# Optimization experiments

Hardware: AMD Instinct MI355X
Metric: run time of the kernel (lower is better)

The kernel has to match this reference:

```python
import jax, jax.numpy as jnp
import numpy as np

B, N, E, H = 4, 2048, 512, 8
D = E // H  # head dim = 64


def setup_inputs() -> dict:
    key = jax.random.key(0)
    ks = jax.random.split(key, 5)
    s = 1.0 / np.sqrt(E)
    return {
        "x": jax.random.normal(ks[0], (B, N, E), dtype=jnp.float32),
        "Wk": jax.random.normal(ks[1], (E, E), dtype=jnp.float32) * s,
        "bk": jax.random.normal(ks[2], (E,), dtype=jnp.float32) * s,
        "Wv": jax.random.normal(ks[3], (E, E), dtype=jnp.float32) * s,
        "bv": jax.random.normal(ks[4], (E,), dtype=jnp.float32) * s,
    }


def reference(x, Wk, bk, Wv, bv):
    b, n, e = x.shape
    # Linear projections (torch Linear: y = x @ W.T + b), split into heads.
    keys = (x @ Wk.T + bk).reshape(b, n, H, D).transpose(0, 2, 1, 3)    # b h n d
    values = (x @ Wv.T + bv).reshape(b, n, H, D).transpose(0, 2, 1, 3)  # b h n d
    # Q = K self-attention: scores [b, h, n, n]
    dotprod = jnp.einsum('bhnd,bhmd->bhnm', keys, keys)
    # softmax over last axis, then unusual POST-softmax scaling by sqrt(emb)
    att = jax.nn.softmax(dotprod, axis=-1) / jnp.sqrt(jnp.asarray(e, x.dtype))
    # dropout p=0 -> identity
    out = jnp.einsum('bhnm,bhmd->bhnd', att, values)
    return out.transpose(0, 2, 1, 3).reshape(b, n, e)
```

## Files before the change

kernel.cpp:

```cpp
#include <hip/hip_runtime.h>

typedef __bf16 bf16_t;
typedef bf16_t bf16x8 __attribute__((ext_vector_type(8)));
typedef float f32x4 __attribute__((ext_vector_type(4)));

#define NSEQ 2048
#define EMB 512
#define HEADS 8
#define HD 64
#define BATCH 4
#define LOG2E 1.4426950408889634f

#define XELEMS (BATCH * NSEQ * EMB)
#define WELEMS (EMB * EMB)

#define MFMA16(a, b, c) __builtin_amdgcn_mfma_f32_16x16x32_bf16(a, b, c, 0, 0, 0)


__global__ __launch_bounds__(256) void convert_kernel(
    const float* __restrict__ x, const float* __restrict__ Wk,
    const float* __restrict__ Wv, bf16_t* __restrict__ xb)
{
  const int i = blockIdx.x * 256 + threadIdx.x;
  const float* src;
  size_t off;
  bf16_t* dst;
  if (i < XELEMS / 8) {
    off = (size_t)i * 8;
    src = x;
    dst = xb + off;
  } else {
    const size_t e = (size_t)(i - XELEMS / 8) * 8;
    if (e < WELEMS) { src = Wk; off = e; }
    else            { src = Wv; off = e - WELEMS; }
    dst = xb + XELEMS + e;
  }
  const float4 a = *(const float4*)(src + off);
  const float4 b = *(const float4*)(src + off + 4);
  bf16x8 v;
  v[0] = (bf16_t)a.x; v[1] = (bf16_t)a.y; v[2] = (bf16_t)a.z; v[3] = (bf16_t)a.w;
  v[4] = (bf16_t)b.x; v[5] = (bf16_t)b.y; v[6] = (bf16_t)b.z; v[7] = (bf16_t)b.w;
  *(bf16x8*)dst = v;
}

__global__ __launch_bounds__(256, 2) void proj_kernel(
    const bf16_t* __restrict__ xb, const bf16_t* __restrict__ Wb,
    const float* __restrict__ bk, const float* __restrict__ bv,
    bf16_t* __restrict__ Kf, bf16_t* __restrict__ Vf)
{
  __shared__ union {
    struct {
      __align__(16) bf16_t A[128 * 64];
      __align__(16) bf16_t B[128 * 64];
    } s;
    __align__(16) bf16_t T[128][136];
  } u;

  const int t    = threadIdx.x;
  const int w    = t >> 6;
  const int lane = t & 63;
  const int quad = lane >> 4;
  const int l15  = lane & 15;
  const int wr   = w >> 1, wc = w & 1;
  const int m0   = blockIdx.x * 128;
  const int n0   = blockIdx.y * 128;
  const int zz   = (blockIdx.y >= 4);

  const int rsub = lane >> 3;
  const int cswz = (lane & 7) ^ rsub;

  auto stage = [&](int it) {
    const int kb = it * 64;
#pragma unroll
    for (int g = 0; g < 4; ++g) {
      const int r = w * 32 + g * 8;
      const bf16_t* gA = xb + (size_t)(m0 + r + rsub) * EMB + kb + cswz * 8;
      const bf16_t* gB = Wb + (size_t)(n0 + r + rsub) * EMB + kb + cswz * 8;
      __builtin_amdgcn_global_load_lds(
          (const __attribute__((address_space(1))) void*)gA,
          (__attribute__((address_space(3))) void*)&u.s.A[r * 64], 16, 0, 0);
      __builtin_amdgcn_global_load_lds(
          (const __attribute__((address_space(1))) void*)gB,
          (__attribute__((address_space(3))) void*)&u.s.B[r * 64], 16, 0, 0);
    }
  };
  auto rdA = [&](int R, int c) {
    return *(const bf16x8*)(&u.s.A[R * 64 + ((c ^ (R & 7)) << 3)]);
  };
  auto rdB = [&](int R, int c) {
    return *(const bf16x8*)(&u.s.B[R * 64 + ((c ^ (R & 7)) << 3)]);
  };

  f32x4 acc[4][4] = {};

  for (int it = 0; it < 8; ++it) {
    stage(it);
    __syncthreads();

    bf16x8 af[4][2], bfr[4][2];
#pragma unroll
    for (int mt = 0; mt < 4; ++mt)
#pragma unroll
      for (int kk = 0; kk < 2; ++kk)
        af[mt][kk] = rdA(wr * 64 + mt * 16 + l15, kk * 4 + quad);
#pragma unroll
    for (int nt = 0; nt < 4; ++nt)
#pragma unroll
      for (int kk = 0; kk < 2; ++kk)
        bfr[nt][kk] = rdB(wc * 64 + nt * 16 + l15, kk * 4 + quad);
#pragma unroll
    for (int kk = 0; kk < 2; ++kk)
#pragma unroll
      for (int mt = 0; mt < 4; ++mt)
#pragma unroll
        for (int nt = 0; nt < 4; ++nt)
          acc[mt][nt] = MFMA16(af[mt][kk], bfr[nt][kk], acc[mt][nt]);

    __syncthreads();
  }

#pragma unroll
  for (int mt = 0; mt < 4; ++mt) {
#pragma unroll
    for (int nt = 0; nt < 4; ++nt) {
      const int F = wc * 64 + nt * 16 + l15;
      const int c = n0 + F;
      const float bb = zz ? bv[c - 512] : bk[c];
#pragma unroll
      for (int reg = 0; reg < 4; ++reg) {
        const int R = wr * 64 + mt * 16 + quad * 4 + reg;
        const float v = acc[mt][nt][reg] + bb;
        if (!zz) u.T[R][F] = (bf16_t)v;
        else     u.T[F][R] = (bf16_t)v;
      }
    }
  }
  __syncthreads();

  if (!zz) {
#pragma unroll
    for (int i = 0; i < 8; ++i) {
      const int fi  = i * 4 + w;
      const int hL  = fi >> 4, kk = (fi >> 3) & 1, ktl = fi & 7;
      const bf16x8 v = *(const bf16x8*)(&u.T[ktl * 16 + l15][hL * 64 + kk * 32 + quad * 8]);
      const int gr = m0 + ktl * 16 + l15;
      const int b = gr >> 11, n = gr & (NSEQ - 1);
      const int bh = b * HEADS + (n0 >> 6) + hL;
      bf16_t* dst = Kf + (((size_t)(bh * 128 + (n >> 4)) * 2 + kk)) * 512 + lane * 8;
      *(bf16x8*)dst = v;
    }
  } else {
#pragma unroll
    for (int i = 0; i < 8; ++i) {
      const int fi   = i * 4 + w;
      const int hL   = fi >> 4, dt = (fi >> 2) & 3, k32l = fi & 3;
      const bf16_t* Trow = &u.T[hL * 64 + dt * 16 + l15][0];
      const int r0 = k32l * 32 + (quad >> 1) * 16 + (quad & 1) * 4;
      union { uint2 d2[2]; bf16x8 v; } vv;
      vv.d2[0] = *(const uint2*)(Trow + r0);
      vv.d2[1] = *(const uint2*)(Trow + r0 + 8);
      const int gr = m0 + k32l * 32;
      const int b = gr >> 11, n = gr & (NSEQ - 1);
      const int bh = b * HEADS + ((n0 - 512) >> 6) + hL;
      bf16_t* dst = Vf + (((size_t)(bh * 64 + (n >> 5)) * 4 + dt)) * 512 + lane * 8;
      *(bf16x8*)dst = vv.v;
    }
  }
}

__global__ __launch_bounds__(256, 2) void flash_kernel(
    const bf16_t* __restrict__ Kf, const bf16_t* __restrict__ Vf,
    float* __restrict__ out)
{
  __shared__ struct {
    __align__(16) float Cb[2][4096];
    __align__(16) float Lb[2][64][16];
  } u;

  const int t    = threadIdx.x;
  const int w    = t >> 6;
  const int lane = t & 63;
  const int quad = lane >> 4;
  const int l15  = lane & 15;
  const int rh   = w & 1;
  const int kh   = w >> 1;

  const int bh = blockIdx.x;
  const int b  = bh >> 3, h = bh & 7;
  const int rowbase = blockIdx.y * 128 + rh * 64;
  const int qtile   = rowbase >> 4;

  const bf16_t* __restrict__ Kb = Kf + (size_t)bh * 128 * 2 * 512;
  const bf16_t* __restrict__ Vb = Vf + (size_t)bh * 64 * 4 * 512;

  bf16x8 qf[4][2];
#pragma unroll
  for (int nt = 0; nt < 4; ++nt)
#pragma unroll
    for (int kk = 0; kk < 2; ++kk)
      qf[nt][kk] = *(const bf16x8*)(Kb + ((size_t)(qtile + nt) * 2 + kk) * 512 + lane * 8);

  float mlog[4];
#pragma unroll
  for (int nt = 0; nt < 4; ++nt) {
    float ss = 0.f;
#pragma unroll
    for (int kk = 0; kk < 2; ++kk)
#pragma unroll
      for (int j = 0; j < 8; ++j) {
        const float qv = (float)qf[nt][kk][j];
        ss = fmaf(qv, qv, ss);
      }
    ss += __shfl_xor(ss, 16, 64);
    ss += __shfl_xor(ss, 32, 64);
    mlog[nt] = ss * LOG2E;
  }

  bf16x8 ones;
#pragma unroll
  for (int j = 0; j < 8; ++j) ones[j] = (bf16_t)1.0f;

  f32x4 acco[4][4] = {};
  f32x4 accll[4]   = {};

  auto load_k = [&](int kt, bf16x8 (&dst)[2][2]) {
    const int kb = kt * 4 + kh * 2;
#pragma unroll
    for (int jt = 0; jt < 2; ++jt)
#pragma unroll
      for (int kk = 0; kk < 2; ++kk)
        dst[jt][kk] =
            *(const bf16x8*)(Kb + ((size_t)(kb + jt) * 2 + kk) * 512 + lane * 8);
  };

  auto body = [&](int kt, bf16x8 (&kcur)[2][2], bf16x8 (&knxt)[2][2]) {
    bf16x8 vf[4];
    const int v32 = kt * 2 + kh;
#pragma unroll
    for (int dt = 0; dt < 4; ++dt)
      vf[dt] = *(const bf16x8*)(Vb + ((size_t)v32 * 4 + dt) * 512 + lane * 8);

    f32x4 st[2][4] = {};
    __builtin_amdgcn_s_setprio(1);
#pragma unroll
    for (int kk = 0; kk < 2; ++kk)
#pragma unroll
      for (int jt = 0; jt < 2; ++jt)
#pragma unroll
        for (int nt = 0; nt < 4; ++nt)
          st[jt][nt] = MFMA16(kcur[jt][kk], qf[nt][kk], st[jt][nt]);
    __builtin_amdgcn_s_setprio(0);

    load_k(kt + 1 < NSEQ / 64 ? kt + 1 : kt, knxt);

    bf16x8 pf[4];
#pragma unroll
    for (int nt = 0; nt < 4; ++nt) {
      union { bf16_t h[2]; unsigned uu; } w00, w01, w10, w11;
      w00.h[0] = (bf16_t)__builtin_amdgcn_exp2f(fmaf(st[0][nt][0], LOG2E, -mlog[nt]));
      w00.h[1] = (bf16_t)__builtin_amdgcn_exp2f(fmaf(st[0][nt][1], LOG2E, -mlog[nt]));
      w01.h[0] = (bf16_t)__builtin_amdgcn_exp2f(fmaf(st[0][nt][2], LOG2E, -mlog[nt]));
      w01.h[1] = (bf16_t)__builtin_amdgcn_exp2f(fmaf(st[0][nt][3], LOG2E, -mlog[nt]));
      w10.h[0] = (bf16_t)__builtin_amdgcn_exp2f(fmaf(st[1][nt][0], LOG2E, -mlog[nt]));
      w10.h[1] = (bf16_t)__builtin_amdgcn_exp2f(fmaf(st[1][nt][1], LOG2E, -mlog[nt]));
      w11.h[0] = (bf16_t)__builtin_amdgcn_exp2f(fmaf(st[1][nt][2], LOG2E, -mlog[nt]));
      w11.h[1] = (bf16_t)__builtin_amdgcn_exp2f(fmaf(st[1][nt][3], LOG2E, -mlog[nt]));
      auto r0 = __builtin_amdgcn_permlane32_swap(w00.uu, w10.uu, false, false);
      auto r1 = __builtin_amdgcn_permlane32_swap(w01.uu, w11.uu, false, false);
      union { unsigned uw[4]; bf16x8 v; } pk;
      pk.uw[0] = r0[0]; pk.uw[1] = r1[0]; pk.uw[2] = r0[1]; pk.uw[3] = r1[1];
      pf[nt] = pk.v;
    }

    __builtin_amdgcn_s_setprio(1);
#pragma unroll
    for (int rt = 0; rt < 4; ++rt) {
      accll[rt] = MFMA16(pf[rt], ones, accll[rt]);
#pragma unroll
      for (int dt = 0; dt < 4; ++dt)
        acco[rt][dt] = MFMA16(pf[rt], vf[dt], acco[rt][dt]);
    }
    __builtin_amdgcn_s_setprio(0);
  };

  bf16x8 kA[2][2], kB[2][2];
  load_k(0, kA);
  for (int kt = 0; kt < NSEQ / 64; kt += 2) {
    body(kt,     kA, kB);
    body(kt + 1, kB, kA);
  }

  __syncthreads();
  if (kh == 1) {
#pragma unroll
    for (int rt = 0; rt < 4; ++rt) {
#pragma unroll
      for (int dt = 0; dt < 4; ++dt)
        *(f32x4*)(&u.Cb[rh][((rt * 4 + dt) * 64 + lane) * 4]) = acco[rt][dt];
      *(f32x4*)(&u.Lb[rh][lane][rt * 4]) = accll[rt];
    }
  }
  __syncthreads();
  if (kh == 0) {
#pragma unroll
    for (int rt = 0; rt < 4; ++rt) {
#pragma unroll
      for (int dt = 0; dt < 4; ++dt)
        acco[rt][dt] += *(const f32x4*)(&u.Cb[rh][((rt * 4 + dt) * 64 + lane) * 4]);
      accll[rt] += *(const f32x4*)(&u.Lb[rh][lane][rt * 4]);
    }

    const float SCL = 0.044194173824159216f;
#pragma unroll
    for (int rt = 0; rt < 4; ++rt)
#pragma unroll
      for (int reg = 0; reg < 4; ++reg) {
        const float f = SCL / accll[rt][reg];
        const int n = rowbase + rt * 16 + quad * 4 + reg;
#pragma unroll
        for (int dt = 0; dt < 4; ++dt)
          out[((size_t)(b * NSEQ + n)) * EMB + h * HD + dt * 16 + l15] =
              acco[rt][dt][reg] * f;
      }
  }
}

extern "C" void kernel_launch(void* const* d_in, const int* in_sizes, int n_in,
                              void* d_out, int out_size, void* d_ws, size_t ws_size,
                              hipStream_t stream) {
  const float* x  = (const float*)d_in[0];
  const float* Wk = (const float*)d_in[1];
  const float* bk = (const float*)d_in[2];
  const float* Wv = (const float*)d_in[3];
  const float* bv = (const float*)d_in[4];
  float* out = (float*)d_out;

  bf16_t* Kf = (bf16_t*)d_ws;
  bf16_t* Vf = Kf + (size_t)BATCH * HEADS * NSEQ * HD;

  bf16_t* xb = (bf16_t*)d_out;
  bf16_t* Wb = xb + XELEMS;

  convert_kernel<<<(XELEMS / 8 + 2 * WELEMS / 8) / 256, 256, 0, stream>>>(
      x, Wk, Wv, xb);

  dim3 pg(8192 / 128, 1024 / 128);
  proj_kernel<<<pg, 256, 0, stream>>>(xb, Wb, bk, bv, Kf, Vf);

  dim3 fg(BATCH * HEADS, NSEQ / 128);
  flash_kernel<<<fg, 256, 0, stream>>>(Kf, Vf, out);
}
```

Baseline: 131.0 us.

## Split flash keys across four waves per block and double-buffer projection tiles

The attention kernel now gives each block 64 query rows and has its four waves each process a quarter of the key sequence. Partial outputs and row sums are combined through shared memory in a two-step tree reduction, the grid is doubled, and the occupancy hint is raised to four blocks per SM. The goal is more concurrent blocks and better latency hiding. Separately, the projection GEMM double-buffers its LDS tiles so the next K-slice loads while the current one is multiplied. The tighter launch bound may cap registers and cause spills, and the reduction adds extra barriers.

```diff
diff --git a/kernel.cpp b/kernel.cpp
--- a/kernel.cpp
+++ b/kernel.cpp
@@ -50,8 +50,8 @@
 {
   __shared__ union {
     struct {
-      __align__(16) bf16_t A[128 * 64];
-      __align__(16) bf16_t B[128 * 64];
+      __align__(16) bf16_t A[2][128 * 64];
+      __align__(16) bf16_t B[2][128 * 64];
     } s;
     __align__(16) bf16_t T[128][136];
   } u;
@@ -69,7 +69,7 @@
   const int rsub = lane >> 3;
   const int cswz = (lane & 7) ^ rsub;
 
-  auto stage = [&](int it) {
+  auto stage = [&](int it, int bufi) {
     const int kb = it * 64;
 #pragma unroll
     for (int g = 0; g < 4; ++g) {
@@ -78,36 +78,39 @@
       const bf16_t* gB = Wb + (size_t)(n0 + r + rsub) * EMB + kb + cswz * 8;
       __builtin_amdgcn_global_load_lds(
           (const __attribute__((address_space(1))) void*)gA,
-          (__attribute__((address_space(3))) void*)&u.s.A[r * 64], 16, 0, 0);
+          (__attribute__((address_space(3))) void*)&u.s.A[bufi][r * 64], 16, 0, 0);
       __builtin_amdgcn_global_load_lds(
           (const __attribute__((address_space(1))) void*)gB,
-          (__attribute__((address_space(3))) void*)&u.s.B[r * 64], 16, 0, 0);
-    }
-  };
-  auto rdA = [&](int R, int c) {
-    return *(const bf16x8*)(&u.s.A[R * 64 + ((c ^ (R & 7)) << 3)]);
-  };
-  auto rdB = [&](int R, int c) {
-    return *(const bf16x8*)(&u.s.B[R * 64 + ((c ^ (R & 7)) << 3)]);
+          (__attribute__((address_space(3))) void*)&u.s.B[bufi][r * 64], 16, 0, 0);
+    }
+  };
+  auto rdA = [&](int bufi, int R, int c) {
+    return *(const bf16x8*)(&u.s.A[bufi][R * 64 + ((c ^ (R & 7)) << 3)]);
+  };
+  auto rdB = [&](int bufi, int R, int c) {
+    return *(const bf16x8*)(&u.s.B[bufi][R * 64 + ((c ^ (R & 7)) << 3)]);
   };
 
   f32x4 acc[4][4] = {};
 
+  stage(0, 0);
+  __syncthreads();
+
   for (int it = 0; it < 8; ++it) {
-    stage(it);
-    __syncthreads();
+    const int cur = it & 1;
+    if (it < 7) stage(it + 1, cur ^ 1);
 
     bf16x8 af[4][2], bfr[4][2];
 #pragma unroll
     for (int mt = 0; mt < 4; ++mt)
 #pragma unroll
       for (int kk = 0; kk < 2; ++kk)
-        af[mt][kk] = rdA(wr * 64 + mt * 16 + l15, kk * 4 + quad);
+        af[mt][kk] = rdA(cur, wr * 64 + mt * 16 + l15, kk * 4 + quad);
 #pragma unroll
     for (int nt = 0; nt < 4; ++nt)
 #pragma unroll
       for (int kk = 0; kk < 2; ++kk)
-        bfr[nt][kk] = rdB(wc * 64 + nt * 16 + l15, kk * 4 + quad);
+        bfr[nt][kk] = rdB(cur, wc * 64 + nt * 16 + l15, kk * 4 + quad);
 #pragma unroll
     for (int kk = 0; kk < 2; ++kk)
 #pragma unroll
@@ -168,7 +171,7 @@
   }
 }
 
-__global__ __launch_bounds__(256, 2) void flash_kernel(
+__global__ __launch_bounds__(256, 4) void flash_kernel(
     const bf16_t* __restrict__ Kf, const bf16_t* __restrict__ Vf,
     float* __restrict__ out)
 {
@@ -178,16 +181,14 @@
   } u;
 
   const int t    = threadIdx.x;
-  const int w    = t >> 6;
+  const int kq   = t >> 6;
   const int lane = t & 63;
   const int quad = lane >> 4;
   const int l15  = lane & 15;
-  const int rh   = w & 1;
-  const int kh   = w >> 1;
 
   const int bh = blockIdx.x;
   const int b  = bh >> 3, h = bh & 7;
-  const int rowbase = blockIdx.y * 128 + rh * 64;
+  const int rowbase = blockIdx.y * 64;
   const int qtile   = rowbase >> 4;
 
   const bf16_t* __restrict__ Kb = Kf + (size_t)bh * 128 * 2 * 512;
@@ -223,8 +224,8 @@
   f32x4 acco[4][4] = {};
   f32x4 accll[4]   = {};
 
-  auto load_k = [&](int kt, bf16x8 (&dst)[2][2]) {
-    const int kb = kt * 4 + kh * 2;
+  auto load_k = [&](int s, bf16x8 (&dst)[2][2]) {
+    const int kb = (kq * 16 + s) * 2;
 #pragma unroll
     for (int jt = 0; jt < 2; ++jt)
 #pragma unroll
@@ -233,9 +234,9 @@
             *(const bf16x8*)(Kb + ((size_t)(kb + jt) * 2 + kk) * 512 + lane * 8);
   };
 
-  auto body = [&](int kt, bf16x8 (&kcur)[2][2], bf16x8 (&knxt)[2][2]) {
+  auto body = [&](int s, bf16x8 (&kcur)[2][2], bf16x8 (&knxt)[2][2]) {
     bf16x8 vf[4];
-    const int v32 = kt * 2 + kh;
+    const int v32 = kq * 16 + s;
 #pragma unroll
     for (int dt = 0; dt < 4; ++dt)
       vf[dt] = *(const bf16x8*)(Vb + ((size_t)v32 * 4 + dt) * 512 + lane * 8);
@@ -251,7 +252,7 @@
           st[jt][nt] = MFMA16(kcur[jt][kk], qf[nt][kk], st[jt][nt]);
     __builtin_amdgcn_s_setprio(0);
 
-    load_k(kt + 1 < NSEQ / 64 ? kt + 1 : kt, knxt);
+    load_k(s + 1 < 16 ? s + 1 : s, knxt);
 
     bf16x8 pf[4];
 #pragma unroll
@@ -285,30 +286,39 @@
 
   bf16x8 kA[2][2], kB[2][2];
   load_k(0, kA);
-  for (int kt = 0; kt < NSEQ / 64; kt += 2) {
-    body(kt,     kA, kB);
-    body(kt + 1, kB, kA);
-  }
-
-  __syncthreads();
-  if (kh == 1) {
+  for (int s = 0; s < 16; s += 2) {
+    body(s,     kA, kB);
+    body(s + 1, kB, kA);
+  }
+
+  auto dump = [&](int slot) {
 #pragma unroll
     for (int rt = 0; rt < 4; ++rt) {
 #pragma unroll
       for (int dt = 0; dt < 4; ++dt)
-        *(f32x4*)(&u.Cb[rh][((rt * 4 + dt) * 64 + lane) * 4]) = acco[rt][dt];
-      *(f32x4*)(&u.Lb[rh][lane][rt * 4]) = accll[rt];
-    }
-  }
-  __syncthreads();
-  if (kh == 0) {
+        *(f32x4*)(&u.Cb[slot][((rt * 4 + dt) * 64 + lane) * 4]) = acco[rt][dt];
+      *(f32x4*)(&u.Lb[slot][lane][rt * 4]) = accll[rt];
+    }
+  };
+  auto gather = [&](int slot) {
 #pragma unroll
     for (int rt = 0; rt < 4; ++rt) {
 #pragma unroll
       for (int dt = 0; dt < 4; ++dt)
-        acco[rt][dt] += *(const f32x4*)(&u.Cb[rh][((rt * 4 + dt) * 64 + lane) * 4]);
-      accll[rt] += *(const f32x4*)(&u.Lb[rh][lane][rt * 4]);
-    }
+        acco[rt][dt] += *(const f32x4*)(&u.Cb[slot][((rt * 4 + dt) * 64 + lane) * 4]);
+      accll[rt] += *(const f32x4*)(&u.Lb[slot][lane][rt * 4]);
+    }
+  };
+
+  __syncthreads();
+  if (kq & 1) dump(kq >> 1);
+  __syncthreads();
+  if (!(kq & 1)) gather(kq >> 1);
+  __syncthreads();
+  if (kq == 2) dump(0);
+  __syncthreads();
+  if (kq == 0) {
+    gather(0);
 
     const float SCL = 0.044194173824159216f;
 #pragma unroll
@@ -347,6 +357,6 @@
   dim3 pg(8192 / 128, 1024 / 128);
   proj_kernel<<<pg, 256, 0, stream>>>(xb, Wb, bk, bv, Kf, Vf);
 
-  dim3 fg(BATCH * HEADS, NSEQ / 128);
+  dim3 fg(BATCH * HEADS, NSEQ / 64);
   flash_kernel<<<fg, 256, 0, stream>>>(Kf, Vf, out);
 }
```

Result: slower. 458.7 us (+250.1%).

## Prefetch projection tiles into registers and use padded LDS layout

Applied to the files above, without the earlier changes.

Swaps the direct global-to-LDS async loads with XOR swizzle for register prefetching. The next K-slice is loaded into registers while MFMAs run on the current one, then stored into a padded [2][128][40] LDS layout that avoids bank conflicts. This overlaps global load latency with compute inside the projection GEMM. In exchange it uses more registers and adds explicit LDS store instructions, which could lower occupancy.

```diff
diff --git a/kernel.cpp b/kernel.cpp
--- a/kernel.cpp
+++ b/kernel.cpp
@@ -50,8 +50,8 @@
 {
   __shared__ union {
     struct {
-      __align__(16) bf16_t A[128 * 64];
-      __align__(16) bf16_t B[128 * 64];
+      __align__(16) bf16_t A[2][128][40];
+      __align__(16) bf16_t B[2][128][40];
     } s;
     __align__(16) bf16_t T[128][136];
   } u;
@@ -66,58 +66,53 @@
   const int n0   = blockIdx.y * 128;
   const int zz   = (blockIdx.y >= 4);
 
-  const int rsub = lane >> 3;
-  const int cswz = (lane & 7) ^ rsub;
-
-  auto stage = [&](int it) {
-    const int kb = it * 64;
-#pragma unroll
-    for (int g = 0; g < 4; ++g) {
-      const int r = w * 32 + g * 8;
-      const bf16_t* gA = xb + (size_t)(m0 + r + rsub) * EMB + kb + cswz * 8;
-      const bf16_t* gB = Wb + (size_t)(n0 + r + rsub) * EMB + kb + cswz * 8;
-      __builtin_amdgcn_global_load_lds(
-          (const __attribute__((address_space(1))) void*)gA,
-          (__attribute__((address_space(3))) void*)&u.s.A[r * 64], 16, 0, 0);
-      __builtin_amdgcn_global_load_lds(
-          (const __attribute__((address_space(1))) void*)gB,
-          (__attribute__((address_space(3))) void*)&u.s.B[r * 64], 16, 0, 0);
+  const int sr = t >> 3;
+  const int sj = t & 7;
+  const int sb = sj >> 2, sc = (sj & 3) * 8;
+
+  bf16x8 pa[4], pb[4];
+  auto prefetch = [&](int k0) {
+#pragma unroll
+    for (int i = 0; i < 4; ++i) {
+      pa[i] = *(const bf16x8*)(xb + (size_t)(m0 + sr + i * 32) * EMB + k0 + sj * 8);
+      pb[i] = *(const bf16x8*)(Wb + (size_t)(n0 + sr + i * 32) * EMB + k0 + sj * 8);
     }
   };
-  auto rdA = [&](int R, int c) {
-    return *(const bf16x8*)(&u.s.A[R * 64 + ((c ^ (R & 7)) << 3)]);
-  };
-  auto rdB = [&](int R, int c) {
-    return *(const bf16x8*)(&u.s.B[R * 64 + ((c ^ (R & 7)) << 3)]);
-  };
 
   f32x4 acc[4][4] = {};
+  prefetch(0);
 
   for (int it = 0; it < 8; ++it) {
-    stage(it);
     __syncthreads();
-
-    bf16x8 af[4][2], bfr[4][2];
+#pragma unroll
+    for (int i = 0; i < 4; ++i) {
+      *(bf16x8*)(&u.s.A[sb][sr + i * 32][sc]) = pa[i];
+      *(bf16x8*)(&u.s.B[sb][sr + i * 32][sc]) = pb[i];
+    }
+    __syncthreads();
+    if (it < 7) prefetch((it + 1) * 64);
+
+    bf16x8 af[4][2], bf[4][2];
 #pragma unroll
     for (int mt = 0; mt < 4; ++mt)
 #pragma unroll
       for (int kk = 0; kk < 2; ++kk)
-        af[mt][kk] = rdA(wr * 64 + mt * 16 + l15, kk * 4 + quad);
+        af[mt][kk] = *(const bf16x8*)(&u.s.A[kk][wr * 64 + mt * 16 + l15][quad * 8]);
 #pragma unroll
     for (int nt = 0; nt < 4; ++nt)
 #pragma unroll
       for (int kk = 0; kk < 2; ++kk)
-        bfr[nt][kk] = rdB(wc * 64 + nt * 16 + l15, kk * 4 + quad);
+        bf[nt][kk] = *(const bf16x8*)(&u.s.B[kk][wc * 64 + nt * 16 + l15][quad * 8]);
 #pragma unroll
     for (int kk = 0; kk < 2; ++kk)
 #pragma unroll
       for (int mt = 0; mt < 4; ++mt)
 #pragma unroll
         for (int nt = 0; nt < 4; ++nt)
-          acc[mt][nt] = MFMA16(af[mt][kk], bfr[nt][kk], acc[mt][nt]);
-
-    __syncthreads();
-  }
+          acc[mt][nt] = MFMA16(af[mt][kk], bf[nt][kk], acc[mt][nt]);
+  }
+
+  __syncthreads();
 
 #pragma unroll
   for (int mt = 0; mt < 4; ++mt) {
```

Result: no change. 131.5 us (+0.4%).
